# Kernel optimization log

Hardware: AMD Instinct MI355X
Metric: run time of the kernel (lower is better)

The kernel has to match this reference:

```python
import jax, jax.numpy as jnp
import numpy as np

N_ENTS = 50000
NUM_RELS = 250   # 2*NUM_RELS with inverses
H = 256
T = 4
E = 200000
M = 200000
L = 2            # num_hidden_layers
RRELU_SLOPE = (1.0/8.0 + 1.0/3.0) / 2.0  # F.rrelu eval-mode negative slope


def _l2n(x):
    # torch F.normalize(dim=1): x / max(||x||_2, eps)
    return x / jnp.maximum(jnp.linalg.norm(x, axis=-1, keepdims=True), 1e-12)


def _rrelu(x):
    return jnp.where(x >= 0, x, RRELU_SLOPE * x)


def setup_inputs() -> dict:
    key = jax.random.key(0)
    ks = jax.random.split(key, 16)
    s = 1.0 / np.sqrt(H)
    inp = {
        'src': jax.random.randint(ks[0], (T, E), 0, N_ENTS, dtype=jnp.int32),
        'dst': jax.random.randint(ks[1], (T, E), 0, N_ENTS, dtype=jnp.int32),
        'etype': jax.random.randint(ks[2], (T, E), 0, 2 * NUM_RELS, dtype=jnp.int32),
        'r2e_ent': jax.random.randint(ks[3], (T, M), 0, N_ENTS, dtype=jnp.int32),
        'r2e_rel': jax.random.randint(ks[4], (T, M), 0, 2 * NUM_RELS, dtype=jnp.int32),
        'dynamic_emb': jax.random.normal(ks[5], (N_ENTS, H), jnp.float32),
        'emb_rel': jax.random.normal(ks[6], (2 * NUM_RELS, H), jnp.float32) * s,
        'w_neighbor': jax.random.normal(ks[7], (L, H, H), jnp.float32) * s,
        'loop_w': jax.random.normal(ks[8], (L, H, H), jnp.float32) * s,
        'evolve_w': jax.random.normal(ks[9], (L, H, H), jnp.float32) * s,
        'gru_w_ih': jax.random.normal(ks[10], (3 * H, 2 * H), jnp.float32) * s,
        'gru_w_hh': jax.random.normal(ks[11], (3 * H, H), jnp.float32) * s,
        'gru_b_ih': jax.random.normal(ks[12], (3 * H,), jnp.float32) * s,
        'gru_b_hh': jax.random.normal(ks[13], (3 * H,), jnp.float32) * s,
    }
    return inp


def reference(src, dst, etype, r2e_ent, r2e_rel, dynamic_emb, emb_rel,
              w_neighbor, loop_w, evolve_w, gru_w_ih, gru_w_hh, gru_b_ih, gru_b_hh):
    n_ents, h_dim = dynamic_emb.shape
    num_r2 = emb_rel.shape[0]
    n_layers = w_neighbor.shape[0]
    t_steps = src.shape[0]

    h = _l2n(dynamic_emb)          # layer_norm=True -> F.normalize
    h0 = emb_rel                    # GRU hidden init at first step
    hist, rels = [], []
    for t in range(t_steps):
        # relation-wise mean of associated entity embeddings (r_to_e grouping)
        te = h[r2e_ent[t]]                                              # [M, H]
        seg = jax.ops.segment_sum(te, r2e_rel[t], num_segments=num_r2)
        cnt = jax.ops.segment_sum(jnp.ones((te.shape[0],), te.dtype), r2e_rel[t], num_segments=num_r2)
        x_in = seg / jnp.maximum(cnt, 1.0)[:, None]                     # zeros for unseen rels
        # GRUCell update of relation embeddings
        x = jnp.concatenate([emb_rel, x_in], axis=1)                    # [2R, 2H]
        gx = x @ gru_w_ih.T + gru_b_ih
        gh = h0 @ gru_w_hh.T + gru_b_hh
        xr, xz, xn = jnp.split(gx, 3, axis=1)
        hr, hz, hn = jnp.split(gh, 3, axis=1)
        r = jax.nn.sigmoid(xr + hr)
        z = jax.nn.sigmoid(xz + hz)
        n = jnp.tanh(xn + r * hn)
        h0 = _l2n((1.0 - z) * n + z * h0)
        rels.append(h0)
        # UnionRGCNLayer stack (gather -> (h_src + rel) @ W -> scatter-sum -> norm + self-loop -> rrelu)
        deg = jax.ops.segment_sum(jnp.ones((src.shape[1],), h.dtype), dst[t], num_segments=n_ents)
        norm = 1.0 / jnp.maximum(deg, 1.0)
        has_in = (deg > 0)[:, None]
        hc = h
        for l in range(n_layers):
            msg = (hc[src[t]] + h0[etype[t]]) @ w_neighbor[l]           # [E, H]
            agg = jax.ops.segment_sum(msg, dst[t], num_segments=n_ents)
            loop = jnp.where(has_in, hc @ loop_w[l], hc @ evolve_w[l])
            hc = _rrelu(agg * norm[:, None] + loop)
        h = _l2n(hc)
        hist.append(h)
    return jnp.stack(hist), jnp.stack(rels)
```

## Files before the change

### kernel.cpp

```cpp
#include <hip/hip_runtime.h>

#define N_ENTS 50000
#define R2 500
#define H 256
#define TSTEPS 4
#define NE 200000
#define NM 200000
#define NL 2
#define SLOPE 0.22916666666666666f
#define SCAN_NB ((N_ENTS + 255) / 256)
#define CPAD 16

typedef __attribute__((ext_vector_type(8))) short short8;
typedef __attribute__((ext_vector_type(4))) short short4v;
typedef __attribute__((ext_vector_type(4))) float f32x4;

static __device__ __forceinline__ float b2f(short s) {
  unsigned u = ((unsigned)(unsigned short)s) << 16;
  return __builtin_bit_cast(float, u);
}
static __device__ __forceinline__ short f2b(float f) {
  unsigned u = __builtin_bit_cast(unsigned, f);
  u = (u + 0x7FFFu + ((u >> 16) & 1u)) >> 16;
  return (short)(unsigned short)u;
}

static __device__ __forceinline__ void gload16(const short* g, short* l) {
  __builtin_amdgcn_global_load_lds(
      (const __attribute__((address_space(1))) void*)g,
      (__attribute__((address_space(3))) void*)l, 16, 0, 0);
}

template<int EPI>
__global__ __launch_bounds__(256, 2)
void gemm_big(const short* __restrict__ A, int lda,
              const short* __restrict__ Bt, int ldb,
              int M, int K,
              float* __restrict__ Cf, int ldc,
              short* __restrict__ Obf, int ldo)
{
  __shared__ short As[128 * 64];
  __shared__ short Bs[256 * 64];
  const int tid = threadIdx.x;
  const int w = tid >> 6, lane = tid & 63;
  const int fr = lane & 15, fq = lane >> 4;
  const int rowh = w >> 1, colh = w & 1;
  const int blk0 = blockIdx.x * 128;
  const int l8 = lane >> 3, s7 = lane & 7;

  f32x4 acc[4][8];
#pragma unroll
  for (int m = 0; m < 4; ++m)
#pragma unroll
    for (int n = 0; n < 8; ++n) {
      acc[m][n][0] = 0.f; acc[m][n][1] = 0.f; acc[m][n][2] = 0.f; acc[m][n][3] = 0.f;
    }

  for (int kc = 0; kc < K; kc += 64) {
    __syncthreads();
#pragma unroll
    for (int i = 0; i < 4; ++i) {
      int row = w * 32 + i * 8 + l8;
      int grow = min(blk0 + row, M - 1);
      const short* g = A + (size_t)grow * lda + kc + ((s7 ^ (row & 7)) << 3);
      gload16(g, As + w * 2048 + i * 512);
    }
#pragma unroll
    for (int i = 0; i < 8; ++i) {
      int row = w * 64 + i * 8 + l8;
      const short* g = Bt + (size_t)row * ldb + kc + ((s7 ^ (row & 7)) << 3);
      gload16(g, Bs + w * 4096 + i * 512);
    }
    __syncthreads();
#pragma unroll
    for (int ks = 0; ks < 2; ++ks) {
      const int sl = ((((ks << 2) | fq) ^ s7) << 3);
      short8 a[4], b[8];
#pragma unroll
      for (int m = 0; m < 4; ++m)
        a[m] = *(const short8*)&As[(rowh * 64 + m * 16 + fr) * 64 + sl];
#pragma unroll
      for (int n = 0; n < 8; ++n)
        b[n] = *(const short8*)&Bs[(colh * 128 + n * 16 + fr) * 64 + sl];
#pragma unroll
      for (int m = 0; m < 4; ++m)
#pragma unroll
        for (int n = 0; n < 8; ++n)
          acc[m][n] = __builtin_amdgcn_mfma_f32_16x16x32_bf16(a[m], b[n], acc[m][n], 0, 0, 0);
    }
  }

  if (EPI == 1) {
#pragma unroll
    for (int m = 0; m < 4; ++m)
#pragma unroll
      for (int n = 0; n < 8; ++n) {
        const int col = colh * 128 + n * 16 + fr;
#pragma unroll
        for (int j = 0; j < 4; ++j) {
          const int r = blk0 + rowh * 64 + m * 16 + fq * 4 + j;
          if (r < M) {
            float v = acc[m][n][j];
            v = v >= 0.f ? v : v * SLOPE;
            Obf[(size_t)r * ldo + col] = f2b(v);
          }
        }
      }
  } else {
    float ss[4][4];
#pragma unroll
    for (int m = 0; m < 4; ++m)
#pragma unroll
      for (int j = 0; j < 4; ++j) ss[m][j] = 0.f;
#pragma unroll
    for (int m = 0; m < 4; ++m)
#pragma unroll
      for (int n = 0; n < 8; ++n)
#pragma unroll
        for (int j = 0; j < 4; ++j) {
          float v = acc[m][n][j];
          v = v >= 0.f ? v : v * SLOPE;
          acc[m][n][j] = v;
          ss[m][j] += v * v;
        }
#pragma unroll
    for (int m = 0; m < 4; ++m)
#pragma unroll
      for (int j = 0; j < 4; ++j) {
        float s = ss[m][j];
        s += __shfl_xor(s, 1, 64);
        s += __shfl_xor(s, 2, 64);
        s += __shfl_xor(s, 4, 64);
        s += __shfl_xor(s, 8, 64);
        ss[m][j] = s;
      }
    __syncthreads();
    float* red = (float*)Bs;
    if (colh == 0 && fr == 0) {
#pragma unroll
      for (int m = 0; m < 4; ++m)
#pragma unroll
        for (int j = 0; j < 4; ++j)
          red[rowh * 128 + m * 16 + fq * 4 + j] = ss[m][j];
    }
    __syncthreads();
    float inv[4][4];
    if (colh == 1) {
#pragma unroll
      for (int m = 0; m < 4; ++m)
#pragma unroll
        for (int j = 0; j < 4; ++j) {
          float tot = ss[m][j] + red[rowh * 128 + m * 16 + fq * 4 + j];
          inv[m][j] = 1.f / fmaxf(sqrtf(tot), 1e-12f);
        }
      if (fr == 0) {
#pragma unroll
        for (int m = 0; m < 4; ++m)
#pragma unroll
          for (int j = 0; j < 4; ++j)
            red[256 + rowh * 128 + m * 16 + fq * 4 + j] = inv[m][j];
      }
    }
    __syncthreads();
    if (colh == 0) {
#pragma unroll
      for (int m = 0; m < 4; ++m)
#pragma unroll
        for (int j = 0; j < 4; ++j)
          inv[m][j] = red[256 + rowh * 128 + m * 16 + fq * 4 + j];
    }
#pragma unroll
    for (int m = 0; m < 4; ++m)
#pragma unroll
      for (int n = 0; n < 8; ++n) {
        const int col = colh * 128 + n * 16 + fr;
#pragma unroll
        for (int j = 0; j < 4; ++j) {
          const int r = blk0 + rowh * 64 + m * 16 + fq * 4 + j;
          if (r < M) {
            float v = acc[m][n][j] * inv[m][j];
            Cf[(size_t)r * ldc + col] = v;
            if (Obf) Obf[(size_t)r * ldo + col] = f2b(v);
          }
        }
      }
  }
}

__global__ __launch_bounds__(256)
void gemm_k(const short* __restrict__ A, int lda,
            const short* __restrict__ Bt, int ldb,
            int M, int K,
            float* __restrict__ Cf, int ldc,
            const float* __restrict__ bias)
{
  __shared__ short bt[256 * 72];
  const int tid = threadIdx.x;
  const int w = tid >> 6;
  const int lane = tid & 63;
  const int fr = lane & 15;
  const int fq = lane >> 4;
  const int col0 = blockIdx.y << 8;
  const int rowbase = blockIdx.x * 64 + w * 16;
  const int arow = min(rowbase + fr, M - 1);
  const long abase = (long)arow * lda + fq * 8;

  f32x4 acc[16];
#pragma unroll
  for (int i = 0; i < 16; ++i) { acc[i][0] = 0.f; acc[i][1] = 0.f; acc[i][2] = 0.f; acc[i][3] = 0.f; }

  for (int kc = 0; kc < K; kc += 64) {
    __syncthreads();
    {
      const short* g = Bt + (long)(col0 + tid) * ldb + kc;
      short* l = &bt[tid * 72];
#pragma unroll
      for (int i = 0; i < 8; ++i)
        *(short8*)(l + i * 8) = *(const short8*)(g + i * 8);
    }
    __syncthreads();
#pragma unroll
    for (int ks = 0; ks < 2; ++ks) {
      short8 a = *(const short8*)(A + abase + kc + ks * 32);
#pragma unroll
      for (int ct = 0; ct < 16; ++ct) {
        short8 b = *(const short8*)&bt[(ct * 16 + fr) * 72 + ks * 32 + fq * 8];
        acc[ct] = __builtin_amdgcn_mfma_f32_16x16x32_bf16(a, b, acc[ct], 0, 0, 0);
      }
    }
  }

  const int crow = rowbase + fq * 4;
#pragma unroll
  for (int ct = 0; ct < 16; ++ct) {
    const int gcol = col0 + ct * 16 + fr;
#pragma unroll
    for (int j = 0; j < 4; ++j) {
      const int r = crow + j;
      if (r < M) {
        float v = acc[ct][j];
        if (bias) v += bias[gcol];
        Cf[(long)r * ldc + gcol] = v;
      }
    }
  }
}

__global__ __launch_bounds__(256)
void gru2_k(const short* __restrict__ x_inb, const short* __restrict__ h0b,
            const short* __restrict__ wihb, const short* __restrict__ whhb,
            const float* __restrict__ gxbase, const float* __restrict__ bhh,
            float* __restrict__ gx, float* __restrict__ gh)
{
  const short* A;  const short* Bt;  int ldb;
  float* Cf;  const float* Cadd;  const float* bias;
  if (blockIdx.z == 0) { A = x_inb; Bt = wihb + 256; ldb = 512; Cf = gx; Cadd = gxbase; bias = nullptr; }
  else                 { A = h0b;   Bt = whhb;       ldb = 256; Cf = gh; Cadd = nullptr; bias = bhh; }

  __shared__ short bt[256 * 72];
  const int tid = threadIdx.x;
  const int w = tid >> 6;
  const int lane = tid & 63;
  const int fr = lane & 15;
  const int fq = lane >> 4;
  const int col0 = blockIdx.y << 8;
  const int rowbase = blockIdx.x * 64 + w * 16;
  const int arow = min(rowbase + fr, R2 - 1);
  const long abase = (long)arow * 256 + fq * 8;

  f32x4 acc[16];
#pragma unroll
  for (int i = 0; i < 16; ++i) { acc[i][0] = 0.f; acc[i][1] = 0.f; acc[i][2] = 0.f; acc[i][3] = 0.f; }

  for (int kc = 0; kc < 256; kc += 64) {
    __syncthreads();
    {
      const short* g = Bt + (long)(col0 + tid) * ldb + kc;
      short* l = &bt[tid * 72];
#pragma unroll
      for (int i = 0; i < 8; ++i)
        *(short8*)(l + i * 8) = *(const short8*)(g + i * 8);
    }
    __syncthreads();
#pragma unroll
    for (int ks = 0; ks < 2; ++ks) {
      short8 a = *(const short8*)(A + abase + kc + ks * 32);
#pragma unroll
      for (int ct = 0; ct < 16; ++ct) {
        short8 b = *(const short8*)&bt[(ct * 16 + fr) * 72 + ks * 32 + fq * 8];
        acc[ct] = __builtin_amdgcn_mfma_f32_16x16x32_bf16(a, b, acc[ct], 0, 0, 0);
      }
    }
  }

  const int crow = rowbase + fq * 4;
#pragma unroll
  for (int ct = 0; ct < 16; ++ct) {
    const int gcol = col0 + ct * 16 + fr;
#pragma unroll
    for (int j = 0; j < 4; ++j) {
      const int r = crow + j;
      if (r < R2) {
        float v = acc[ct][j];
        if (Cadd) v += Cadd[(long)r * 768 + gcol];
        if (bias) v += bias[gcol];
        Cf[(long)r * 768 + gcol] = v;
      }
    }
  }
}

__global__ __launch_bounds__(256)
void l2init_k(const float* __restrict__ de, short* __restrict__ hb)
{
  const int w = threadIdx.x >> 6, lane = threadIdx.x & 63;
  const int row = blockIdx.x * 4 + w;
  f32x4 v = *(const f32x4*)&de[(long)row * H + lane * 4];
  float s = v[0]*v[0] + v[1]*v[1] + v[2]*v[2] + v[3]*v[3];
  s += __shfl_xor(s, 1, 64);  s += __shfl_xor(s, 2, 64);
  s += __shfl_xor(s, 4, 64);  s += __shfl_xor(s, 8, 64);
  s += __shfl_xor(s, 16, 64); s += __shfl_xor(s, 32, 64);
  float sc = 1.f / fmaxf(sqrtf(s), 1e-12f);
  short4v o;
  o[0] = f2b(v[0]*sc); o[1] = f2b(v[1]*sc); o[2] = f2b(v[2]*sc); o[3] = f2b(v[3]*sc);
  *(short4v*)&hb[(long)row * 512 + lane * 4] = o;
}

__global__ __launch_bounds__(256)
void prep_k(const float* __restrict__ wn, const float* __restrict__ lw,
            const float* __restrict__ ew, const float* __restrict__ wih,
            const float* __restrict__ whh, const float* __restrict__ erel,
            short* __restrict__ wcatb, short* __restrict__ evt,
            short* __restrict__ wihb, short* __restrict__ whhb,
            short* __restrict__ erelb, float* __restrict__ h0, short* __restrict__ h0b)
{
  long i = (long)blockIdx.x * 256 + threadIdx.x;
  if (i < (long)NL * 256 * 512) {
    int l = (int)(i / (256 * 512));
    int rem = (int)(i % (256 * 512));
    int j = rem / 512;
    int k = rem % 512;
    float v = (k < 256) ? wn[(long)l * 65536 + k * 256 + j]
                        : lw[(long)l * 65536 + (k - 256) * 256 + j];
    wcatb[i] = f2b(v);
    return;
  }
  i -= (long)NL * 256 * 512;
  if (i < (long)NL * 65536) {
    int l = (int)(i >> 16);
    int rem = (int)(i & 65535);
    int c = rem >> 8, k = rem & 255;
    evt[i] = f2b(ew[(long)l * 65536 + k * 256 + c]);
    return;
  }
  i -= (long)NL * 65536;
  if (i < 768 * 512) { wihb[i] = f2b(wih[i]); return; }
  i -= 768 * 512;
  if (i < 768 * 256) { whhb[i] = f2b(whh[i]); return; }
  i -= 768 * 256;
  if (i < (long)R2 * H) {
    float v = erel[i];
    erelb[i] = f2b(v); h0[i] = v; h0b[i] = f2b(v);
  }
}
#define PREP_N ((long)NL * 256 * 512 + (long)NL * 65536 + 768 * 512 + 768 * 256 + (long)R2 * H)

__global__ __launch_bounds__(256)
void zero_all_k(unsigned* __restrict__ deg, unsigned* __restrict__ curd,
                unsigned* __restrict__ cnt, unsigned* __restrict__ cur,
                unsigned* __restrict__ nz, unsigned* __restrict__ flags)
{
  const int t = blockIdx.y;
  int i = blockIdx.x * 256 + threadIdx.x;
  if (i < N_ENTS) { deg[(long)t * N_ENTS + i] = 0u; curd[(long)t * N_ENTS + i] = 0u; }
  if (i < R2) { cnt[((long)t * R2 + i) * CPAD] = 0u; cur[((long)t * R2 + i) * CPAD] = 0u; }
  if (i < SCAN_NB) flags[t * SCAN_NB + i] = 0u;
  if (i == 0) nz[t * CPAD] = 0u;
}

__global__ __launch_bounds__(256)
void count_all_k(const int* __restrict__ relA, const int* __restrict__ dstA,
                 unsigned* __restrict__ cntA, unsigned* __restrict__ degA)
{
  const int t = blockIdx.y;
  const int* rel = relA + (long)t * NM;
  const int* dstv = dstA + (long)t * NE;
  unsigned* cnt = cntA + (long)t * R2 * CPAD;
  unsigned* deg = degA + (long)t * N_ENTS;
  __shared__ unsigned lh[R2];
  for (int i = threadIdx.x; i < R2; i += 256) lh[i] = 0;
  __syncthreads();
  for (long i = (long)blockIdx.x * 256 + threadIdx.x; i < NM; i += (long)gridDim.x * 256)
    atomicAdd(&lh[rel[i]], 1u);
  for (long i = (long)blockIdx.x * 256 + threadIdx.x; i < NE; i += (long)gridDim.x * 256)
    atomicAdd(&deg[dstv[i]], 1u);
  __syncthreads();
  for (int i = threadIdx.x; i < R2; i += 256)
    if (lh[i]) atomicAdd(&cnt[i * CPAD], lh[i]);
}

__global__ __launch_bounds__(256)
void scan_all_k(const unsigned* __restrict__ degA, unsigned* __restrict__ offdA,
                unsigned* __restrict__ flagsA,
                unsigned* __restrict__ zlA, unsigned* __restrict__ nzA,
                const unsigned* __restrict__ cntA, unsigned* __restrict__ offA)
{
  const int t = blockIdx.y;
  if (blockIdx.x == SCAN_NB) {
    const unsigned* cnt = cntA + (long)t * R2 * CPAD;
    unsigned* off = offA + t * (R2 + 1);
    __shared__ unsigned sr[512];
    const int tt = threadIdx.x;
    sr[tt] = (tt < R2) ? cnt[tt * CPAD] : 0u;
    sr[tt + 256] = (tt + 256 < R2) ? cnt[(tt + 256) * CPAD] : 0u;
    __syncthreads();
#pragma unroll
    for (int d = 1; d < 512; d <<= 1) {
      unsigned v0 = (tt >= d) ? sr[tt - d] : 0u;
      unsigned v1 = (tt + 256 >= d) ? sr[tt + 256 - d] : 0u;
      __syncthreads();
      sr[tt] += v0; sr[tt + 256] += v1;
      __syncthreads();
    }
    if (tt < R2) off[tt] = (tt == 0) ? 0u : sr[tt - 1];
    if (tt + 256 < R2) off[tt + 256] = sr[tt + 255];
    if (tt == 0) off[R2] = sr[R2 - 1];
    return;
  }
  const unsigned* deg = degA + (long)t * N_ENTS;
  unsigned* offd = offdA + (long)t * (N_ENTS + 1);
  unsigned* flags = flagsA + t * SCAN_NB;
  unsigned* zl = zlA + (long)t * N_ENTS;
  unsigned* nz = nzA + t * CPAD;
  __shared__ unsigned s[256];
  __shared__ unsigned sexc;
  const int tid = threadIdx.x;
  const int b = blockIdx.x;
  const int i = b * 256 + tid;
  unsigned v = (i < N_ENTS) ? deg[i] : 0u;
  s[tid] = v;
  __syncthreads();
#pragma unroll
  for (int d = 1; d < 256; d <<= 1) {
    unsigned t2 = (tid >= d) ? s[tid - d] : 0u;
    __syncthreads();
    s[tid] += t2;
    __syncthreads();
  }
  const unsigned total = s[255];
  if (tid == 0) {
    if (b == 0) {
      __threadfence();
      atomicExch(&flags[0], (2u << 30) | total);
      sexc = 0u;
    } else {
      __threadfence();
      atomicExch(&flags[b], (1u << 30) | total);
      unsigned exc = 0u;
      int j = b - 1;
      while (j >= 0) {
        unsigned f;
        do { f = atomicAdd(&flags[j], 0u); } while ((f >> 30) == 0u);
        exc += f & 0x3FFFFFFFu;
        if ((f >> 30) == 2u) break;
        --j;
      }
      __threadfence();
      atomicExch(&flags[b], (2u << 30) | (exc + total));
      sexc = exc;
    }
  }
  __syncthreads();
  const unsigned exc = sexc;
  if (i < N_ENTS) {
    offd[i] = exc + s[tid] - v;
    if (v == 0u) { unsigned p2 = atomicAdd(nz, 1u); zl[p2] = i; }
  }
  if (i == 0) offd[N_ENTS] = NE;
}

__global__ __launch_bounds__(256)
void scatter_all_k(const int* __restrict__ relA, const int* __restrict__ entA,
                   const unsigned* __restrict__ offA, unsigned* __restrict__ curA,
                   int* __restrict__ seA,
                   const int* __restrict__ srcA, const int* __restrict__ dstA,
                   const int* __restrict__ etA, const unsigned* __restrict__ offdA,
                   unsigned* __restrict__ curdA, int2* __restrict__ se2A)
{
  const int t = blockIdx.y;
  if (blockIdx.x < 256) {
    const int* rel = relA + (long)t * NM;
    const int* ent = entA + (long)t * NM;
    const unsigned* off = offA + t * (R2 + 1);
    unsigned* cur = curA + (long)t * R2 * CPAD;
    int* se = seA + (long)t * NM;
    for (long i = (long)blockIdx.x * 256 + threadIdx.x; i < NM; i += 256l * 256) {
      int r = rel[i];
      unsigned p = atomicAdd(&cur[r * CPAD], 1u);
      se[off[r] + p] = ent[i];
    }
  } else {
    const int* srcv = srcA + (long)t * NE;
    const int* dstv = dstA + (long)t * NE;
    const int* etv = etA + (long)t * NE;
    const unsigned* offd = offdA + (long)t * (N_ENTS + 1);
    unsigned* curd = curdA + (long)t * N_ENTS;
    int2* se2 = se2A + (long)t * NE;
    for (long i = (long)(blockIdx.x - 256) * 256 + threadIdx.x; i < NE; i += 512l * 256) {
      int d = dstv[i];
      unsigned p = atomicAdd(&curd[d], 1u);
      se2[offd[d] + p] = make_int2(srcv[i], etv[i]);
    }
  }
}

__global__ __launch_bounds__(256)
void segpart_k(const unsigned* __restrict__ off, const int* __restrict__ se,
               const short* __restrict__ hb, float* __restrict__ xinf)
{
  __shared__ float red[4][256];
  const int r = blockIdx.x >> 2, s = blockIdx.x & 3;
  const int w = threadIdx.x >> 6, lane = threadIdx.x & 63;
  const int half = lane >> 5, sl = lane & 31;
  const unsigned b = off[r], e = off[r + 1], len = e - b;
  const unsigned lo = b + ((len * s) >> 2), hi = b + ((len * (s + 1)) >> 2);
  float a[8];
#pragma unroll
  for (int j = 0; j < 8; ++j) a[j] = 0.f;
  unsigned i = lo + w * 2;
  for (; i + 10 <= hi; i += 16) {
    int e0 = se[i + half];
    int e1 = se[i + 8 + half];
    short8 h0v = *(const short8*)&hb[(long)e0 * 512 + sl * 8];
    short8 h1v = *(const short8*)&hb[(long)e1 * 512 + sl * 8];
#pragma unroll
    for (int j = 0; j < 8; ++j) a[j] += b2f(h0v[j]) + b2f(h1v[j]);
  }
  for (; i + 2 <= hi; i += 8) {
    int e0 = se[i + half];
    short8 hv = *(const short8*)&hb[(long)e0 * 512 + sl * 8];
#pragma unroll
    for (int j = 0; j < 8; ++j) a[j] += b2f(hv[j]);
  }
  if (i + half < hi) {
    int e0 = se[i + half];
    short8 hv = *(const short8*)&hb[(long)e0 * 512 + sl * 8];
#pragma unroll
    for (int j = 0; j < 8; ++j) a[j] += b2f(hv[j]);
  }
#pragma unroll
  for (int j = 0; j < 8; ++j) a[j] += __shfl_xor(a[j], 32, 64);
  if (half == 0) {
#pragma unroll
    for (int j = 0; j < 8; ++j) red[w][sl * 8 + j] = a[j];
  }
  __syncthreads();
  const int t = threadIdx.x;
  xinf[((long)s * R2 + r) * 256 + t] =
      (red[0][t] + red[1][t]) + (red[2][t] + red[3][t]);
}

__global__ __launch_bounds__(256)
void segfin_k(const float* __restrict__ xinf, const unsigned* __restrict__ cnt,
              short* __restrict__ x_inb)
{
  const int r = blockIdx.x, tid = threadIdx.x;
  float v = xinf[(long)r * 256 + tid] + xinf[((long)R2 + r) * 256 + tid]
          + xinf[((long)2 * R2 + r) * 256 + tid] + xinf[((long)3 * R2 + r) * 256 + tid];
  v /= fmaxf((float)cnt[r * CPAD], 1.f);
  x_inb[(long)r * 256 + tid] = f2b(v);
}

__global__ __launch_bounds__(256)
void gate_k(const float* __restrict__ gx, const float* __restrict__ gh,
            float* __restrict__ h0, short* __restrict__ h0b, float* __restrict__ relout)
{
  __shared__ float red[4];
  const int r = blockIdx.x, c = threadIdx.x;
  const long b = (long)r * 768;
  float xr = gx[b + c], xz = gx[b + 256 + c], xn = gx[b + 512 + c];
  float hr = gh[b + c], hz = gh[b + 256 + c], hn = gh[b + 512 + c];
  float rr = 1.f / (1.f + expf(-(xr + hr)));
  float z  = 1.f / (1.f + expf(-(xz + hz)));
  float nn = tanhf(xn + rr * hn);
  float v = (1.f - z) * nn + z * h0[(long)r * H + c];
  float s = v * v;
  s += __shfl_xor(s, 1, 64);  s += __shfl_xor(s, 2, 64);
  s += __shfl_xor(s, 4, 64);  s += __shfl_xor(s, 8, 64);
  s += __shfl_xor(s, 16, 64); s += __shfl_xor(s, 32, 64);
  const int w = c >> 6;
  if ((c & 63) == 0) red[w] = s;
  __syncthreads();
  float tot = (red[0] + red[1]) + (red[2] + red[3]);
  float sc = 1.f / fmaxf(sqrtf(tot), 1e-12f);
  v *= sc;
  h0[(long)r * H + c] = v;
  h0b[(long)r * H + c] = f2b(v);
  relout[(long)r * H + c] = v;
}

__global__ __launch_bounds__(256)
void agg_first_k(const int2* __restrict__ se2, const unsigned* __restrict__ offd,
                 const short* __restrict__ hb, const short* __restrict__ h0b,
                 short* __restrict__ rsum, short* __restrict__ acat)
{
  const int w = threadIdx.x >> 6, lane = threadIdx.x & 63;
  const int half = lane >> 5, sl = lane & 31;
  const int row = blockIdx.x * 4 + w;
  const unsigned b = offd[row], e = offd[row + 1];
  float ha[8], ra[8];
#pragma unroll
  for (int j = 0; j < 8; ++j) { ha[j] = 0.f; ra[j] = 0.f; }
  unsigned i = b;
  for (; i + 4 <= e; i += 4) {
    int2 e0 = se2[i + half];
    int2 e1 = se2[i + 2 + half];
    short8 h0v = *(const short8*)&hb[(long)e0.x * 512 + sl * 8];
    short8 r0v = *(const short8*)&h0b[(long)e0.y * 256 + sl * 8];
    short8 h1v = *(const short8*)&hb[(long)e1.x * 512 + sl * 8];
    short8 r1v = *(const short8*)&h0b[(long)e1.y * 256 + sl * 8];
#pragma unroll
    for (int j = 0; j < 8; ++j) {
      ha[j] += b2f(h0v[j]) + b2f(h1v[j]);
      ra[j] += b2f(r0v[j]) + b2f(r1v[j]);
    }
  }
  for (; i < e; i += 2) {
    if (i + half < e) {
      int2 e0 = se2[i + half];
      short8 hv = *(const short8*)&hb[(long)e0.x * 512 + sl * 8];
      short8 rv = *(const short8*)&h0b[(long)e0.y * 256 + sl * 8];
#pragma unroll
      for (int j = 0; j < 8; ++j) { ha[j] += b2f(hv[j]); ra[j] += b2f(rv[j]); }
    }
  }
#pragma unroll
  for (int j = 0; j < 8; ++j) {
    ha[j] += __shfl_xor(ha[j], 32, 64);
    ra[j] += __shfl_xor(ra[j], 32, 64);
  }
  if (half == 0) {
    const float nm = 1.f / fmaxf((float)(e - b), 1.f);
    short8 rs, o;
#pragma unroll
    for (int j = 0; j < 8; ++j) {
      rs[j] = f2b(ra[j]);
      o[j] = f2b((ha[j] + ra[j]) * nm);
    }
    *(short8*)&rsum[(long)row * 256 + sl * 8] = rs;
    *(short8*)&acat[(long)row * 512 + sl * 8] = o;
  }
}

__global__ __launch_bounds__(256)
void agg_second_k(const int2* __restrict__ se2, const unsigned* __restrict__ offd,
                  const short* __restrict__ hb, const short* __restrict__ rsum,
                  short* __restrict__ acat)
{
  const int w = threadIdx.x >> 6, lane = threadIdx.x & 63;
  const int half = lane >> 5, sl = lane & 31;
  const int row = blockIdx.x * 4 + w;
  const unsigned b = offd[row], e = offd[row + 1];
  float ha[8];
#pragma unroll
  for (int j = 0; j < 8; ++j) ha[j] = 0.f;
  unsigned i = b;
  for (; i + 4 <= e; i += 4) {
    int2 e0 = se2[i + half];
    int2 e1 = se2[i + 2 + half];
    short8 h0v = *(const short8*)&hb[(long)e0.x * 512 + sl * 8];
    short8 h1v = *(const short8*)&hb[(long)e1.x * 512 + sl * 8];
#pragma unroll
    for (int j = 0; j < 8; ++j) ha[j] += b2f(h0v[j]) + b2f(h1v[j]);
  }
  for (; i < e; i += 2) {
    if (i + half < e) {
      int2 e0 = se2[i + half];
      short8 hv = *(const short8*)&hb[(long)e0.x * 512 + sl * 8];
#pragma unroll
      for (int j = 0; j < 8; ++j) ha[j] += b2f(hv[j]);
    }
  }
#pragma unroll
  for (int j = 0; j < 8; ++j) ha[j] += __shfl_xor(ha[j], 32, 64);
  if (half == 0) {
    short8 rs = *(const short8*)&rsum[(long)row * 256 + sl * 8];
    const float nm = 1.f / fmaxf((float)(e - b), 1.f);
    short8 o;
#pragma unroll
    for (int j = 0; j < 8; ++j) o[j] = f2b((ha[j] + b2f(rs[j])) * nm);
    *(short8*)&acat[(long)row * 512 + sl * 8] = o;
  }
}

template<int FINAL>
__global__ __launch_bounds__(256)
void fixup_k(const unsigned* __restrict__ nz, const unsigned* __restrict__ zl,
             const short* __restrict__ hbc, const short* __restrict__ evt,
             short* __restrict__ hbn, float* __restrict__ outF)
{
  __shared__ float x[H];
  __shared__ float red[4];
  const unsigned n = *nz;
  const short* wrow = evt + (long)threadIdx.x * 256;
  for (unsigned zi = blockIdx.x; zi < n; zi += gridDim.x) {
    const int row = zl[zi];
    __syncthreads();
    x[threadIdx.x] = b2f(hbc[(long)row * 512 + threadIdx.x]);
    __syncthreads();
    float acc = 0.f;
#pragma unroll
    for (int k0 = 0; k0 < H; k0 += 8) {
      short8 wv = *(const short8*)&wrow[k0];
      acc += x[k0]     * b2f(wv[0]) + x[k0 + 1] * b2f(wv[1])
           + x[k0 + 2] * b2f(wv[2]) + x[k0 + 3] * b2f(wv[3])
           + x[k0 + 4] * b2f(wv[4]) + x[k0 + 5] * b2f(wv[5])
           + x[k0 + 6] * b2f(wv[6]) + x[k0 + 7] * b2f(wv[7]);
    }
    float v = acc >= 0.f ? acc : acc * SLOPE;
    if (FINAL) {
      float s = v * v;
      s += __shfl_xor(s, 1, 64);  s += __shfl_xor(s, 2, 64);
      s += __shfl_xor(s, 4, 64);  s += __shfl_xor(s, 8, 64);
      s += __shfl_xor(s, 16, 64); s += __shfl_xor(s, 32, 64);
      const int w = threadIdx.x >> 6;
      if ((threadIdx.x & 63) == 0) red[w] = s;
      __syncthreads();
      float tot = (red[0] + red[1]) + (red[2] + red[3]);
      float sc = 1.f / fmaxf(sqrtf(tot), 1e-12f);
      v *= sc;
      outF[(long)row * H + threadIdx.x] = v;
    }
    if (hbn) hbn[(long)row * 512 + threadIdx.x] = f2b(v);
  }
}

extern "C" void kernel_launch(void* const* d_in, const int* in_sizes, int n_in,
                              void* d_out, int out_size, void* d_ws, size_t ws_size,
                              hipStream_t stream)
{
  (void)in_sizes; (void)n_in; (void)out_size; (void)ws_size;
  const int* src = (const int*)d_in[0];
  const int* dst = (const int*)d_in[1];
  const int* ety = (const int*)d_in[2];
  const int* r2e_ent = (const int*)d_in[3];
  const int* r2e_rel = (const int*)d_in[4];
  const float* dyn = (const float*)d_in[5];
  const float* erel = (const float*)d_in[6];
  const float* wn = (const float*)d_in[7];
  const float* lw = (const float*)d_in[8];
  const float* ew = (const float*)d_in[9];
  const float* wih = (const float*)d_in[10];
  const float* whh = (const float*)d_in[11];
  const float* bih = (const float*)d_in[12];
  const float* bhh = (const float*)d_in[13];

  float* out = (float*)d_out;
  float* hist = out;
  float* rels = out + (long)TSTEPS * N_ENTS * H;

  char* p = (char*)d_ws;
  auto alloc = [&](size_t n) { char* r = p; p += (n + 255) & ~(size_t)255; return r; };
  short*    AcatA  = (short*)alloc((size_t)N_ENTS * 512 * 2);
  short*    AcatB  = (short*)alloc((size_t)N_ENTS * 512 * 2);
  short*    rsum   = (short*)alloc((size_t)N_ENTS * 256 * 2);
  unsigned* deg    = (unsigned*)alloc((size_t)TSTEPS * N_ENTS * 4);
  unsigned* offd   = (unsigned*)alloc((size_t)TSTEPS * (N_ENTS + 1) * 4);
  unsigned* curd   = (unsigned*)alloc((size_t)TSTEPS * N_ENTS * 4);
  unsigned* flags  = (unsigned*)alloc((size_t)TSTEPS * SCAN_NB * 4);
  int2*     se2    = (int2*)alloc((size_t)TSTEPS * NE * 8);
  unsigned* zl     = (unsigned*)alloc((size_t)TSTEPS * N_ENTS * 4);
  unsigned* nz     = (unsigned*)alloc((size_t)TSTEPS * CPAD * 4);
  unsigned* cnt    = (unsigned*)alloc((size_t)TSTEPS * R2 * CPAD * 4);
  unsigned* off    = (unsigned*)alloc((size_t)TSTEPS * (R2 + 1) * 4);
  unsigned* cur    = (unsigned*)alloc((size_t)TSTEPS * R2 * CPAD * 4);
  int*      se     = (int*)alloc((size_t)TSTEPS * NM * 4);
  float*    xinf   = (float*)alloc((size_t)4 * R2 * 256 * 4);
  short*    x_inb  = (short*)alloc((size_t)R2 * H * 2);
  float*    gxbase = (float*)alloc((size_t)R2 * 768 * 4);
  float*    gx     = (float*)alloc((size_t)R2 * 768 * 4);
  float*    gh     = (float*)alloc((size_t)R2 * 768 * 4);
  float*    h0     = (float*)alloc((size_t)R2 * H * 4);
  short*    h0b    = (short*)alloc((size_t)R2 * H * 2);
  short*    erelb  = (short*)alloc((size_t)R2 * H * 2);
  short*    wcatb  = (short*)alloc((size_t)NL * 256 * 512 * 2);
  short*    evt    = (short*)alloc((size_t)NL * H * H * 2);
  short*    wihb   = (short*)alloc((size_t)768 * 512 * 2);
  short*    whhb   = (short*)alloc((size_t)768 * 256 * 2);

  prep_k<<<(int)((PREP_N + 255) / 256), 256, 0, stream>>>(
      wn, lw, ew, wih, whh, erel, wcatb, evt, wihb, whhb, erelb, h0, h0b);
  l2init_k<<<N_ENTS / 4, 256, 0, stream>>>(dyn, AcatA + 256);

  gemm_k<<<dim3(8, 3), 256, 0, stream>>>(erelb, 256, wihb, 512, R2, 256,
                                         gxbase, 768, bih);

  zero_all_k<<<dim3(SCAN_NB, TSTEPS), 256, 0, stream>>>(deg, curd, cnt, cur, nz, flags);
  count_all_k<<<dim3(512, TSTEPS), 256, 0, stream>>>(r2e_rel, dst, cnt, deg);
  scan_all_k<<<dim3(SCAN_NB + 1, TSTEPS), 256, 0, stream>>>(deg, offd, flags, zl, nz, cnt, off);
  scatter_all_k<<<dim3(768, TSTEPS), 256, 0, stream>>>(r2e_rel, r2e_ent, off, cur, se,
                                                       src, dst, ety, offd, curd, se2);

  short* Acur = AcatA;
  short* Anxt = AcatB;

  for (int t = 0; t < TSTEPS; ++t) {
    float* hist_t = hist + (long)t * N_ENTS * H;
    float* rels_t = rels + (long)t * R2 * H;
    const unsigned* off_t  = off + t * (R2 + 1);
    const int*      se_t   = se + (long)t * NM;
    const unsigned* offd_t = offd + (long)t * (N_ENTS + 1);
    const int2*     se2_t  = se2 + (long)t * NE;
    const unsigned* cnt_t  = cnt + (long)t * R2 * CPAD;
    const unsigned* nz_t   = nz + t * CPAD;
    const unsigned* zl_t   = zl + (long)t * N_ENTS;

    segpart_k<<<R2 * 4, 256, 0, stream>>>(off_t, se_t, Acur + 256, xinf);
    segfin_k<<<R2, 256, 0, stream>>>(xinf, cnt_t, x_inb);
    gru2_k<<<dim3(8, 3, 2), 256, 0, stream>>>(x_inb, h0b, wihb, whhb, gxbase, bhh, gx, gh);
    gate_k<<<R2, 256, 0, stream>>>(gx, gh, h0, h0b, rels_t);

    agg_first_k<<<N_ENTS / 4, 256, 0, stream>>>(se2_t, offd_t, Acur + 256, h0b, rsum, Acur);
    gemm_big<1><<<391, 256, 0, stream>>>(Acur, 512, wcatb, 512,
                                         N_ENTS, 512, nullptr, 0, Anxt + 256, 512);
    fixup_k<0><<<512, 256, 0, stream>>>(nz_t, zl_t, Acur + 256, evt, Anxt + 256, nullptr);
    { short* tmp = Acur; Acur = Anxt; Anxt = tmp; }

    agg_second_k<<<N_ENTS / 4, 256, 0, stream>>>(se2_t, offd_t, Acur + 256, rsum, Acur);
    const bool last = (t == TSTEPS - 1);
    gemm_big<2><<<391, 256, 0, stream>>>(Acur, 512, wcatb + 256 * 512, 512,
                                         N_ENTS, 512, hist_t, 256,
                                         last ? nullptr : (Anxt + 256), 512);
    fixup_k<1><<<512, 256, 0, stream>>>(nz_t, zl_t, Acur + 256, evt + (long)H * H,
                                        last ? nullptr : (Anxt + 256), hist_t);
    { short* tmp = Acur; Acur = Anxt; Anxt = tmp; }
  }
}
```

Before: 1.021 ms.

## Fuse zero-degree fixup into GEMM grid and segment finalize into GRU GEMM

Extra blocks are appended to the big GEMM launch to compute the evolve-weight path for zero in-degree rows, and the main GEMM epilogue skips those rows by checking the degree. This removes two fixup kernel launches per timestep and the serial dependency between GEMM and fixup. The segment-mean finalize kernel is removed by having the GRU GEMM sum the four partial sums, scale by the count and convert to bf16 on the fly. The cost is extra global reads in the GRU A-load, an extra shared-memory footprint in gemm_big, and a degree load per row in the epilogue.

```diff
diff --git a/kernel.cpp b/kernel.cpp
--- a/kernel.cpp
+++ b/kernel.cpp
@@ -10,6 +10,8 @@
 #define SLOPE 0.22916666666666666f
 #define SCAN_NB ((N_ENTS + 255) / 256)
 #define CPAD 16
+#define GB_MAIN 391
+#define GB_FIX 64
 
 typedef __attribute__((ext_vector_type(8))) short short8;
 typedef __attribute__((ext_vector_type(4))) short short4v;
@@ -37,11 +39,53 @@
               const short* __restrict__ Bt, int ldb,
               int M, int K,
               float* __restrict__ Cf, int ldc,
-              short* __restrict__ Obf, int ldo)
+              short* __restrict__ Obf, int ldo,
+              const unsigned* __restrict__ degv,
+              const unsigned* __restrict__ nz, const unsigned* __restrict__ zl,
+              const short* __restrict__ evt_l)
 {
   __shared__ short As[128 * 64];
   __shared__ short Bs[256 * 64];
+  __shared__ float xs[H];
+  __shared__ float redf[4];
   const int tid = threadIdx.x;
+
+  if (blockIdx.x >= GB_MAIN) {
+    const unsigned n = *nz;
+    const short* wrow = evt_l + (long)tid * 256;
+    for (unsigned zi = blockIdx.x - GB_MAIN; zi < n; zi += GB_FIX) {
+      const int row = zl[zi];
+      __syncthreads();
+      xs[tid] = b2f(A[(long)row * lda + 256 + tid]);
+      __syncthreads();
+      float acc = 0.f;
+#pragma unroll
+      for (int k0 = 0; k0 < H; k0 += 8) {
+        short8 wv = *(const short8*)&wrow[k0];
+        acc += xs[k0]     * b2f(wv[0]) + xs[k0 + 1] * b2f(wv[1])
+             + xs[k0 + 2] * b2f(wv[2]) + xs[k0 + 3] * b2f(wv[3])
+             + xs[k0 + 4] * b2f(wv[4]) + xs[k0 + 5] * b2f(wv[5])
+             + xs[k0 + 6] * b2f(wv[6]) + xs[k0 + 7] * b2f(wv[7]);
+      }
+      float v = acc >= 0.f ? acc : acc * SLOPE;
+      if (EPI == 2) {
+        float s = v * v;
+        s += __shfl_xor(s, 1, 64);  s += __shfl_xor(s, 2, 64);
+        s += __shfl_xor(s, 4, 64);  s += __shfl_xor(s, 8, 64);
+        s += __shfl_xor(s, 16, 64); s += __shfl_xor(s, 32, 64);
+        const int w = tid >> 6;
+        if ((tid & 63) == 0) redf[w] = s;
+        __syncthreads();
+        float tot = (redf[0] + redf[1]) + (redf[2] + redf[3]);
+        float sc = 1.f / fmaxf(sqrtf(tot), 1e-12f);
+        v *= sc;
+        Cf[(long)row * ldc + tid] = v;
+      }
+      if (Obf) Obf[(long)row * ldo + tid] = f2b(v);
+    }
+    return;
+  }
+
   const int w = tid >> 6, lane = tid & 63;
   const int fr = lane & 15, fq = lane >> 4;
   const int rowh = w >> 1, colh = w & 1;
@@ -94,12 +138,12 @@
 #pragma unroll
     for (int m = 0; m < 4; ++m)
 #pragma unroll
-      for (int n = 0; n < 8; ++n) {
-        const int col = colh * 128 + n * 16 + fr;
-#pragma unroll
-        for (int j = 0; j < 4; ++j) {
-          const int r = blk0 + rowh * 64 + m * 16 + fq * 4 + j;
-          if (r < M) {
+      for (int j = 0; j < 4; ++j) {
+        const int r = blk0 + rowh * 64 + m * 16 + fq * 4 + j;
+        if (r < M && degv[r] != 0u) {
+#pragma unroll
+          for (int n = 0; n < 8; ++n) {
+            const int col = colh * 128 + n * 16 + fr;
             float v = acc[m][n][j];
             v = v >= 0.f ? v : v * SLOPE;
             Obf[(size_t)r * ldo + col] = f2b(v);
@@ -172,12 +216,12 @@
 #pragma unroll
     for (int m = 0; m < 4; ++m)
 #pragma unroll
-      for (int n = 0; n < 8; ++n) {
-        const int col = colh * 128 + n * 16 + fr;
-#pragma unroll
-        for (int j = 0; j < 4; ++j) {
-          const int r = blk0 + rowh * 64 + m * 16 + fq * 4 + j;
-          if (r < M) {
+      for (int j = 0; j < 4; ++j) {
+        const int r = blk0 + rowh * 64 + m * 16 + fq * 4 + j;
+        if (r < M && degv[r] != 0u) {
+#pragma unroll
+          for (int n = 0; n < 8; ++n) {
+            const int col = colh * 128 + n * 16 + fr;
             float v = acc[m][n][j] * inv[m][j];
             Cf[(size_t)r * ldc + col] = v;
             if (Obf) Obf[(size_t)r * ldo + col] = f2b(v);
@@ -247,15 +291,17 @@
 }
 
 __global__ __launch_bounds__(256)
-void gru2_k(const short* __restrict__ x_inb, const short* __restrict__ h0b,
+void gru2_k(const float* __restrict__ xinf, const unsigned* __restrict__ cnt,
+            const short* __restrict__ h0b,
             const short* __restrict__ wihb, const short* __restrict__ whhb,
             const float* __restrict__ gxbase, const float* __restrict__ bhh,
             float* __restrict__ gx, float* __restrict__ gh)
 {
-  const short* A;  const short* Bt;  int ldb;
+  const int z = blockIdx.z;
+  const short* Bt;  int ldb;
   float* Cf;  const float* Cadd;  const float* bias;
-  if (blockIdx.z == 0) { A = x_inb; Bt = wihb + 256; ldb = 512; Cf = gx; Cadd = gxbase; bias = nullptr; }
-  else                 { A = h0b;   Bt = whhb;       ldb = 256; Cf = gh; Cadd = nullptr; bias = bhh; }
+  if (z == 0) { Bt = wihb + 256; ldb = 512; Cf = gx; Cadd = gxbase; bias = nullptr; }
+  else        { Bt = whhb;       ldb = 256; Cf = gh; Cadd = nullptr; bias = bhh; }
 
   __shared__ short bt[256 * 72];
   const int tid = threadIdx.x;
@@ -267,6 +313,8 @@
   const int rowbase = blockIdx.x * 64 + w * 16;
   const int arow = min(rowbase + fr, R2 - 1);
   const long abase = (long)arow * 256 + fq * 8;
+  float invc = 1.f;
+  if (z == 0) invc = 1.f / fmaxf((float)cnt[arow * CPAD], 1.f);
 
   f32x4 acc[16];
 #pragma unroll
@@ -284,7 +332,25 @@
     __syncthreads();
 #pragma unroll
     for (int ks = 0; ks < 2; ++ks) {
-      short8 a = *(const short8*)(A + abase + kc + ks * 32);
+      short8 a;
+      if (z == 0) {
+        const long kb = abase + kc + ks * 32;
+        f32x4 s0 = *(const f32x4*)&xinf[kb];
+        f32x4 s1 = *(const f32x4*)&xinf[(long)R2 * 256 + kb];
+        f32x4 s2 = *(const f32x4*)&xinf[(long)2 * R2 * 256 + kb];
+        f32x4 s3 = *(const f32x4*)&xinf[(long)3 * R2 * 256 + kb];
+        f32x4 t0 = *(const f32x4*)&xinf[kb + 4];
+        f32x4 t1 = *(const f32x4*)&xinf[(long)R2 * 256 + kb + 4];
+        f32x4 t2 = *(const f32x4*)&xinf[(long)2 * R2 * 256 + kb + 4];
+        f32x4 t3 = *(const f32x4*)&xinf[(long)3 * R2 * 256 + kb + 4];
+#pragma unroll
+        for (int j = 0; j < 4; ++j) {
+          a[j]     = f2b(((s0[j] + s1[j]) + (s2[j] + s3[j])) * invc);
+          a[4 + j] = f2b(((t0[j] + t1[j]) + (t2[j] + t3[j])) * invc);
+        }
+      } else {
+        a = *(const short8*)(h0b + abase + kc + ks * 32);
+      }
 #pragma unroll
       for (int ct = 0; ct < 16; ++ct) {
         short8 b = *(const short8*)&bt[(ct * 16 + fr) * 72 + ks * 32 + fq * 8];
@@ -558,17 +624,6 @@
   const int t = threadIdx.x;
   xinf[((long)s * R2 + r) * 256 + t] =
       (red[0][t] + red[1][t]) + (red[2][t] + red[3][t]);
-}
-
-__global__ __launch_bounds__(256)
-void segfin_k(const float* __restrict__ xinf, const unsigned* __restrict__ cnt,
-              short* __restrict__ x_inb)
-{
-  const int r = blockIdx.x, tid = threadIdx.x;
-  float v = xinf[(long)r * 256 + tid] + xinf[((long)R2 + r) * 256 + tid]
-          + xinf[((long)2 * R2 + r) * 256 + tid] + xinf[((long)3 * R2 + r) * 256 + tid];
-  v /= fmaxf((float)cnt[r * CPAD], 1.f);
-  x_inb[(long)r * 256 + tid] = f2b(v);
 }
 
 __global__ __launch_bounds__(256)
@@ -693,48 +748,6 @@
   }
 }
 
-template<int FINAL>
-__global__ __launch_bounds__(256)
-void fixup_k(const unsigned* __restrict__ nz, const unsigned* __restrict__ zl,
-             const short* __restrict__ hbc, const short* __restrict__ evt,
-             short* __restrict__ hbn, float* __restrict__ outF)
-{
-  __shared__ float x[H];
-  __shared__ float red[4];
-  const unsigned n = *nz;
-  const short* wrow = evt + (long)threadIdx.x * 256;
-  for (unsigned zi = blockIdx.x; zi < n; zi += gridDim.x) {
-    const int row = zl[zi];
-    __syncthreads();
-    x[threadIdx.x] = b2f(hbc[(long)row * 512 + threadIdx.x]);
-    __syncthreads();
-    float acc = 0.f;
-#pragma unroll
-    for (int k0 = 0; k0 < H; k0 += 8) {
-      short8 wv = *(const short8*)&wrow[k0];
-      acc += x[k0]     * b2f(wv[0]) + x[k0 + 1] * b2f(wv[1])
-           + x[k0 + 2] * b2f(wv[2]) + x[k0 + 3] * b2f(wv[3])
-           + x[k0 + 4] * b2f(wv[4]) + x[k0 + 5] * b2f(wv[5])
-           + x[k0 + 6] * b2f(wv[6]) + x[k0 + 7] * b2f(wv[7]);
-    }
-    float v = acc >= 0.f ? acc : acc * SLOPE;
-    if (FINAL) {
-      float s = v * v;
-      s += __shfl_xor(s, 1, 64);  s += __shfl_xor(s, 2, 64);
-      s += __shfl_xor(s, 4, 64);  s += __shfl_xor(s, 8, 64);
-      s += __shfl_xor(s, 16, 64); s += __shfl_xor(s, 32, 64);
-      const int w = threadIdx.x >> 6;
-      if ((threadIdx.x & 63) == 0) red[w] = s;
-      __syncthreads();
-      float tot = (red[0] + red[1]) + (red[2] + red[3]);
-      float sc = 1.f / fmaxf(sqrtf(tot), 1e-12f);
-      v *= sc;
-      outF[(long)row * H + threadIdx.x] = v;
-    }
-    if (hbn) hbn[(long)row * 512 + threadIdx.x] = f2b(v);
-  }
-}
-
 extern "C" void kernel_launch(void* const* d_in, const int* in_sizes, int n_in,
                               void* d_out, int out_size, void* d_ws, size_t ws_size,
                               hipStream_t stream)
@@ -776,7 +789,6 @@
   unsigned* cur    = (unsigned*)alloc((size_t)TSTEPS * R2 * CPAD * 4);
   int*      se     = (int*)alloc((size_t)TSTEPS * NM * 4);
   float*    xinf   = (float*)alloc((size_t)4 * R2 * 256 * 4);
-  short*    x_inb  = (short*)alloc((size_t)R2 * H * 2);
   float*    gxbase = (float*)alloc((size_t)R2 * 768 * 4);
   float*    gx     = (float*)alloc((size_t)R2 * 768 * 4);
   float*    gh     = (float*)alloc((size_t)R2 * 768 * 4);
@@ -814,25 +826,25 @@
     const unsigned* cnt_t  = cnt + (long)t * R2 * CPAD;
     const unsigned* nz_t   = nz + t * CPAD;
     const unsigned* zl_t   = zl + (long)t * N_ENTS;
+    const unsigned* deg_t  = deg + (long)t * N_ENTS;
 
     segpart_k<<<R2 * 4, 256, 0, stream>>>(off_t, se_t, Acur + 256, xinf);
-    segfin_k<<<R2, 256, 0, stream>>>(xinf, cnt_t, x_inb);
-    gru2_k<<<dim3(8, 3, 2), 256, 0, stream>>>(x_inb, h0b, wihb, whhb, gxbase, bhh, gx, gh);
+    gru2_k<<<dim3(8, 3, 2), 256, 0, stream>>>(xinf, cnt_t, h0b, wihb, whhb,
+                                              gxbase, bhh, gx, gh);
     gate_k<<<R2, 256, 0, stream>>>(gx, gh, h0, h0b, rels_t);
 
     agg_first_k<<<N_ENTS / 4, 256, 0, stream>>>(se2_t, offd_t, Acur + 256, h0b, rsum, Acur);
-    gemm_big<1><<<391, 256, 0, stream>>>(Acur, 512, wcatb, 512,
-                                         N_ENTS, 512, nullptr, 0, Anxt + 256, 512);
-    fixup_k<0><<<512, 256, 0, stream>>>(nz_t, zl_t, Acur + 256, evt, Anxt + 256, nullptr);
+    gemm_big<1><<<GB_MAIN + GB_FIX, 256, 0, stream>>>(
+        Acur, 512, wcatb, 512, N_ENTS, 512, nullptr, 0, Anxt + 256, 512,
+        deg_t, nz_t, zl_t, evt);
     { short* tmp = Acur; Acur = Anxt; Anxt = tmp; }
 
     agg_second_k<<<N_ENTS / 4, 256, 0, stream>>>(se2_t, offd_t, Acur + 256, rsum, Acur);
     const bool last = (t == TSTEPS - 1);
-    gemm_big<2><<<391, 256, 0, stream>>>(Acur, 512, wcatb + 256 * 512, 512,
-                                         N_ENTS, 512, hist_t, 256,
-                                         last ? nullptr : (Anxt + 256), 512);
-    fixup_k<1><<<512, 256, 0, stream>>>(nz_t, zl_t, Acur + 256, evt + (long)H * H,
-                                        last ? nullptr : (Anxt + 256), hist_t);
+    gemm_big<2><<<GB_MAIN + GB_FIX, 256, 0, stream>>>(
+        Acur, 512, wcatb + 256 * 512, 512, N_ENTS, 512, hist_t, 256,
+        last ? nullptr : (Anxt + 256), 512,
+        deg_t, nz_t, zl_t, evt + (long)H * H);
     { short* tmp = Acur; Acur = Anxt; Anxt = tmp; }
   }
 }
```

Result: slower. 1.338 ms (+31.1%).
